# Kernel optimization log

Measured on AMD Instinct MI355X. Metric: run time of the kernel, lower is better.

## Reference

```python
import jax, jax.numpy as jnp
import numpy as np

DIM = 4096
NUM_HEAD = 32
NUM_KV_HEAD = 8
ROPE_THETA = 10000.0
B, T = 2, 2048


def apply_rope(x, start_pos=0, theta=ROPE_THETA):
    # x: [B, T, H, d_head]; rotate half-split pairs by position-dependent angles
    d = x.shape[-1]
    half = d // 2
    inv_freq = 1.0 / (theta ** (jnp.arange(0, half, dtype=jnp.float32) / half))
    pos = jnp.arange(x.shape[1], dtype=jnp.float32) + start_pos  # [T]
    ang = pos[:, None] * inv_freq[None, :]                       # [T, half]
    cos = jnp.cos(ang)[None, :, None, :]
    sin = jnp.sin(ang)[None, :, None, :]
    x1, x2 = x[..., :half], x[..., half:]
    return jnp.concatenate([x1 * cos - x2 * sin, x1 * sin + x2 * cos], axis=-1)


def setup_inputs() -> dict:
    key = jax.random.key(0)
    ks = jax.random.split(key, 5)
    scale = 0.02
    X = jax.random.normal(ks[0], (B, T, DIM), dtype=jnp.float32)
    Wq = jax.random.normal(ks[1], (DIM, DIM), dtype=jnp.float32) * scale
    Wk = jax.random.normal(ks[2], (DIM, DIM // NUM_HEAD * NUM_KV_HEAD), dtype=jnp.float32) * scale
    Wv = jax.random.normal(ks[3], (DIM, DIM // NUM_HEAD * NUM_KV_HEAD), dtype=jnp.float32) * scale
    Wo = jax.random.normal(ks[4], (DIM, DIM), dtype=jnp.float32) * scale
    return {"X": X, "Wq": Wq, "Wk": Wk, "Wv": Wv, "Wo": Wo}


def reference(X, Wq, Wk, Wv, Wo):
    Bs, Ts, C = X.shape
    H, Hkv = NUM_HEAD, NUM_KV_HEAD
    dh = C // H
    G = H // Hkv  # GQA group size

    Q = apply_rope((X @ Wq).reshape(Bs, Ts, H, dh))      # [B,T,H,dh]
    K = apply_rope((X @ Wk).reshape(Bs, Ts, Hkv, dh))    # [B,T,Hkv,dh]
    V = (X @ Wv).reshape(Bs, Ts, Hkv, dh)                # [B,T,Hkv,dh]

    # [B,Hkv,G,T,dh]: grouped layout equivalent to repeat_interleave on head dim
    Qh = Q.transpose(0, 2, 1, 3).reshape(Bs, Hkv, G, Ts, dh)
    Kh = K.transpose(0, 2, 1, 3)  # [B,Hkv,T,dh]
    Vh = V.transpose(0, 2, 1, 3)

    scores = jnp.einsum('bkgtd,bksd->bkgts', Qh, Kh) / jnp.sqrt(jnp.float32(dh))
    causal = jnp.tril(jnp.ones((Ts, Ts), dtype=bool))
    scores = jnp.where(causal[None, None, None], scores, -jnp.inf)
    attn = jax.nn.softmax(scores, axis=-1)
    out = jnp.einsum('bkgts,bksd->bkgtd', attn, Vh)       # [B,Hkv,G,T,dh]
    out = out.reshape(Bs, H, Ts, dh).transpose(0, 2, 1, 3).reshape(Bs, Ts, C)
    return out @ Wo
```

## Files before the change

kernel.cpp:

```cpp
#include <hip/hip_runtime.h>
#include <hip/hip_bf16.h>
#include <cstdint>
#include <cstddef>

#define B_   2
#define T_   2048
#define DIM_ 4096
#define H_   32
#define HKV_ 8
#define DH_  128
#define MROWS (B_*T_)

typedef __bf16 bf16_t;
typedef bf16_t bf16x8 __attribute__((ext_vector_type(8)));
typedef bf16_t bf16x4 __attribute__((ext_vector_type(4)));
typedef float  f32x4  __attribute__((ext_vector_type(4)));

typedef __attribute__((address_space(1))) void gvoid_t;
typedef __attribute__((address_space(3))) void lvoid_t;

__device__ __forceinline__ void gld_lds16(const void* g, void* l) {
  __builtin_amdgcn_global_load_lds((gvoid_t*)g, (lvoid_t*)l, 16, 0, 0);
}

__device__ __forceinline__ f32x4 mfma16(bf16x8 a, bf16x8 b, f32x4 c) {
  return __builtin_amdgcn_mfma_f32_16x16x32_bf16(a, b, c, 0, 0, 0);
}

__global__ void cast_f32_bf16(const float* __restrict__ in,
                              bf16_t* __restrict__ out, int n4) {
  int i = blockIdx.x * blockDim.x + threadIdx.x;
  if (i < n4) {
    float4 v = ((const float4*)in)[i];
    bf16x4 o;
    o[0] = (bf16_t)v.x; o[1] = (bf16_t)v.y; o[2] = (bf16_t)v.z; o[3] = (bf16_t)v.w;
    ((bf16x4*)out)[i] = o;
  }
}

__global__ void transpose_cast(const float* __restrict__ in,
                               bf16_t* __restrict__ out, int K, int N) {
  __shared__ float tile[32][33];
  int n0 = blockIdx.x * 32, k0 = blockIdx.y * 32;
  int tx = threadIdx.x, ty = threadIdx.y;
#pragma unroll
  for (int j = 0; j < 4; ++j)
    tile[ty + j*8][tx] = in[(size_t)(k0 + ty + j*8) * N + n0 + tx];
  __syncthreads();
#pragma unroll
  for (int j = 0; j < 4; ++j)
    out[(size_t)(n0 + ty + j*8) * K + k0 + tx] = (bf16_t)tile[tx][ty + j*8];
}

template <int OUT_F32>
__global__ __launch_bounds__(256, 2)
void gemm_bt(const bf16_t* __restrict__ A, const bf16_t* __restrict__ BT,
             void* __restrict__ C, int M, int N, int K) {
  __shared__ __align__(16) bf16_t Als[128 * 32];
  __shared__ __align__(16) bf16_t Bls[128 * 32];
  const int tid  = threadIdx.x;
  const int wave = tid >> 6, lane = tid & 63;
  const int quad = lane >> 4, l16 = lane & 15;
  const int wm = wave >> 1, wn = wave & 1;
  const int m0 = blockIdx.y * 128, n0 = blockIdx.x * 128;

  f32x4 acc[4][4] = {};

  const int srow = lane >> 2;
  const int scol = (lane & 3) * 8;

  for (int k0 = 0; k0 < K; k0 += 32) {
#pragma unroll
    for (int c = 0; c < 2; ++c) {
      int ch = wave * 2 + c;
      gld_lds16(A + (size_t)(m0 + ch*16 + srow) * K + k0 + scol,
                &Als[ch*512 + srow*32 + scol]);
    }
#pragma unroll
    for (int c = 0; c < 2; ++c) {
      int ch = wave * 2 + c;
      gld_lds16(BT + (size_t)(n0 + ch*16 + srow) * K + k0 + scol,
                &Bls[ch*512 + srow*32 + scol]);
    }
    __syncthreads();

    bf16x8 af[4], bfr[4];
#pragma unroll
    for (int mi = 0; mi < 4; ++mi)
      af[mi] = *(const bf16x8*)&Als[(wm*64 + mi*16 + l16)*32 + quad*8];
#pragma unroll
    for (int ni = 0; ni < 4; ++ni)
      bfr[ni] = *(const bf16x8*)&Bls[(wn*64 + ni*16 + l16)*32 + quad*8];
#pragma unroll
    for (int mi = 0; mi < 4; ++mi)
#pragma unroll
      for (int ni = 0; ni < 4; ++ni)
        acc[mi][ni] = mfma16(af[mi], bfr[ni], acc[mi][ni]);
    __syncthreads();
  }

#pragma unroll
  for (int mi = 0; mi < 4; ++mi)
#pragma unroll
    for (int ni = 0; ni < 4; ++ni)
#pragma unroll
      for (int r = 0; r < 4; ++r) {
        int row = m0 + wm*64 + mi*16 + quad*4 + r;
        int col = n0 + wn*64 + ni*16 + l16;
        if (OUT_F32)
          ((float*)C)[(size_t)row * N + col] = acc[mi][ni][r];
        else
          ((bf16_t*)C)[(size_t)row * N + col] = (bf16_t)acc[mi][ni][r];
      }
}

__global__ void rope_kernel(bf16_t* __restrict__ X, int Hn, int total) {
  int i = blockIdx.x * blockDim.x + threadIdx.x;
  if (i >= total) return;
  int d   = i & 63;
  int rem = i >> 6;
  int h   = rem % Hn; rem /= Hn;
  int t   = rem % T_;
  int b   = rem / T_;
  size_t base = ((size_t)(b * T_ + t) * Hn + h) * DH_;
  float x1 = (float)X[base + d];
  float x2 = (float)X[base + 64 + d];
  float inv_freq = expf(-(float)d * 0.14391156758f);
  float ang = (float)t * inv_freq;
  float s, c;
  sincosf(ang, &s, &c);
  X[base + d]      = (bf16_t)(x1 * c - x2 * s);
  X[base + 64 + d] = (bf16_t)(x1 * s + x2 * c);
}

__global__ void v_transpose(const bf16_t* __restrict__ Vb,
                            bf16_t* __restrict__ VT) {
  __shared__ bf16_t tile[32][33];
  int t0 = blockIdx.x * 32;
  int d0 = blockIdx.y * 32;
  int bk = blockIdx.z;
  int b = bk >> 3, kv = bk & 7;
  int tx = threadIdx.x, ty = threadIdx.y;
#pragma unroll
  for (int j = 0; j < 4; ++j)
    tile[ty + j*8][tx] =
        Vb[(size_t)(b * T_ + t0 + ty + j*8) * (HKV_*DH_) + kv*DH_ + d0 + tx];
  __syncthreads();
#pragma unroll
  for (int j = 0; j < 4; ++j)
    VT[((size_t)bk * DH_ + d0 + ty + j*8) * T_ + t0 + tx] = tile[tx][ty + j*8];
}

__global__ __launch_bounds__(256, 2)
void flash_attn(const bf16_t* __restrict__ Qb, const bf16_t* __restrict__ Kb,
                const bf16_t* __restrict__ VT, bf16_t* __restrict__ Ob) {
  __shared__ __align__(16) bf16_t Kls[2][64 * 128];
  __shared__ __align__(16) bf16_t Vls[2][128 * 64];
  __shared__ __align__(16) bf16_t Pls[128 * 64];

  const int tid = threadIdx.x, wave = tid >> 6, lane = tid & 63;
  const int quad = lane >> 4, l16 = lane & 15;
  const int qt = (int)gridDim.x - 1 - (int)blockIdx.x;
  const int h = blockIdx.y, b = blockIdx.z;
  const int kv = h >> 2;

  bf16x8 q[2][4];
#pragma unroll
  for (int mi = 0; mi < 2; ++mi) {
    const bf16_t* base =
        Qb + (size_t)(b*T_ + qt*128 + wave*32 + mi*16 + l16) * DIM_ + h*DH_;
#pragma unroll
    for (int kk = 0; kk < 4; ++kk)
      q[mi][kk] = *(const bf16x8*)(base + kk*32 + quad*8);
  }

  float m_st[2][4], l_st[2][4];
  f32x4 o_acc[2][8] = {};
#pragma unroll
  for (int mi = 0; mi < 2; ++mi)
#pragma unroll
    for (int r = 0; r < 4; ++r) { m_st[mi][r] = -1e30f; l_st[mi][r] = 0.f; }

  const int nkv = 2 * (qt + 1);

  auto stage = [&](int kvt, int pb) {
    int r_in = lane >> 4, cph = lane & 15;
#pragma unroll
    for (int c = 0; c < 4; ++c) {
      int ch = wave * 4 + c;
      int krow = ch * 4 + r_in;
      int clog = cph ^ (krow & 7);
      gld_lds16(Kb + (size_t)(b*T_ + kvt*64 + krow) * (HKV_*DH_) + kv*DH_ + clog*8,
                &Kls[pb][ch*512 + lane*8]);
    }
    int r8 = lane >> 3, c8 = lane & 7;
#pragma unroll
    for (int c = 0; c < 4; ++c) {
      int ch = wave * 4 + c;
      int drow = ch * 8 + r8;
      int clog = c8 ^ (drow & 7);
      gld_lds16(VT + ((size_t)(b*HKV_ + kv) * DH_ + drow) * T_ + kvt*64 + clog*8,
                &Vls[pb][ch*512 + lane*8]);
    }
  };

  stage(0, 0);

  const float S2 = 0.08838834764831845f * 1.4426950408889634f;
  const float THRraw = 8.0f / 0.08838834764831845f;

  for (int kvt = 0; kvt < nkv; ++kvt) {
    const int p = kvt & 1;
    __syncthreads();
    if (kvt + 1 < nkv) stage(kvt + 1, p ^ 1);

    f32x4 s[2][4] = {};
    __builtin_amdgcn_s_setprio(1);
#pragma unroll
    for (int kk = 0; kk < 4; ++kk) {
      bf16x8 kf[4];
#pragma unroll
      for (int ni = 0; ni < 4; ++ni) {
        int krow = ni*16 + l16;
        int cphys = (kk*4 + quad) ^ (krow & 7);
        kf[ni] = *(const bf16x8*)&Kls[p][krow*128 + cphys*8];
      }
#pragma unroll
      for (int mi = 0; mi < 2; ++mi)
#pragma unroll
        for (int ni = 0; ni < 4; ++ni)
          s[mi][ni] = mfma16(q[mi][kk], kf[ni], s[mi][ni]);
    }
    __builtin_amdgcn_s_setprio(0);

    const bool need_mask = (kvt >= 2*qt);
#pragma unroll
    for (int mi = 0; mi < 2; ++mi) {
      float mx[4];
#pragma unroll
      for (int r = 0; r < 4; ++r) {
        int rpos = qt*128 + wave*32 + mi*16 + quad*4 + r;
        float m = -1e30f;
#pragma unroll
        for (int ni = 0; ni < 4; ++ni) {
          float v = s[mi][ni][r];
          if (need_mask) {
            int cpos = kvt*64 + ni*16 + l16;
            if (cpos > rpos) v = -1e30f;
          }
          s[mi][ni][r] = v;
          m = fmaxf(m, v);
        }
#pragma unroll
        for (int off = 1; off < 16; off <<= 1)
          m = fmaxf(m, __shfl_xor(m, off, 64));
        mx[r] = m;
      }
      bool defer = true;
#pragma unroll
      for (int r = 0; r < 4; ++r)
        defer = defer && (mx[r] <= m_st[mi][r] + THRraw);
      if (__all(defer)) {
#pragma unroll
        for (int r = 0; r < 4; ++r) {
          float mn2 = m_st[mi][r] * S2;
          float rs = 0.f;
#pragma unroll
          for (int ni = 0; ni < 4; ++ni) {
            float pv = __builtin_amdgcn_exp2f(fmaf(s[mi][ni][r], S2, -mn2));
            s[mi][ni][r] = pv;
            rs += pv;
          }
#pragma unroll
          for (int off = 1; off < 16; off <<= 1)
            rs += __shfl_xor(rs, off, 64);
          l_st[mi][r] += rs;
        }
      } else {
        float al[4];
#pragma unroll
        for (int r = 0; r < 4; ++r) {
          float mnew = fmaxf(m_st[mi][r], mx[r]);
          al[r] = __builtin_amdgcn_exp2f((m_st[mi][r] - mnew) * S2);
          m_st[mi][r] = mnew;
          float mn2 = mnew * S2;
          float rs = 0.f;
#pragma unroll
          for (int ni = 0; ni < 4; ++ni) {
            float pv = __builtin_amdgcn_exp2f(fmaf(s[mi][ni][r], S2, -mn2));
            s[mi][ni][r] = pv;
            rs += pv;
          }
#pragma unroll
          for (int off = 1; off < 16; off <<= 1)
            rs += __shfl_xor(rs, off, 64);
          l_st[mi][r] = l_st[mi][r] * al[r] + rs;
        }
#pragma unroll
        for (int ni = 0; ni < 8; ++ni)
#pragma unroll
          for (int r = 0; r < 4; ++r) o_acc[mi][ni][r] *= al[r];
      }
#pragma unroll
      for (int ni = 0; ni < 4; ++ni)
#pragma unroll
        for (int r = 0; r < 4; ++r) {
          int prow = wave*32 + mi*16 + quad*4 + r;
          int g = (ni*2 + (l16 >> 3)) ^ (prow & 7);
          Pls[prow*64 + g*8 + (l16 & 7)] = (bf16_t)s[mi][ni][r];
        }
    }

    __builtin_amdgcn_s_setprio(1);
#pragma unroll
    for (int kk = 0; kk < 2; ++kk) {
      bf16x8 pf[2], vf[8];
#pragma unroll
      for (int mi = 0; mi < 2; ++mi) {
        int prow = wave*32 + mi*16 + l16;
        int g = (kk*4 + quad) ^ (prow & 7);
        pf[mi] = *(const bf16x8*)&Pls[prow*64 + g*8];
      }
#pragma unroll
      for (int ni = 0; ni < 8; ++ni) {
        int drow = ni*16 + l16;
        int cphys = (kk*4 + quad) ^ (drow & 7);
        vf[ni] = *(const bf16x8*)&Vls[p][drow*64 + cphys*8];
      }
#pragma unroll
      for (int mi = 0; mi < 2; ++mi)
#pragma unroll
        for (int ni = 0; ni < 8; ++ni)
          o_acc[mi][ni] = mfma16(pf[mi], vf[ni], o_acc[mi][ni]);
    }
    __builtin_amdgcn_s_setprio(0);
  }

#pragma unroll
  for (int mi = 0; mi < 2; ++mi) {
    float inv[4];
#pragma unroll
    for (int r = 0; r < 4; ++r) inv[r] = 1.f / l_st[mi][r];
#pragma unroll
    for (int ni = 0; ni < 8; ++ni)
#pragma unroll
      for (int r = 0; r < 4; ++r) {
        size_t row = (size_t)(b*T_ + qt*128 + wave*32 + mi*16 + quad*4 + r);
        int col = h*DH_ + ni*16 + l16;
        Ob[row * DIM_ + col] = (bf16_t)(o_acc[mi][ni][r] * inv[r]);
      }
  }
}

extern "C" void kernel_launch(void* const* d_in, const int* in_sizes, int n_in,
                              void* d_out, int out_size, void* d_ws, size_t ws_size,
                              hipStream_t stream) {
  const float* X  = (const float*)d_in[0];
  const float* Wq = (const float*)d_in[1];
  const float* Wk = (const float*)d_in[2];
  const float* Wv = (const float*)d_in[3];
  const float* Wo = (const float*)d_in[4];
  float* out = (float*)d_out;

  char* ws = (char*)d_ws;
  const size_t SZ_X  = (size_t)MROWS * DIM_ * 2;
  const size_t SZ_WQ = (size_t)DIM_ * DIM_ * 2;
  const size_t SZ_WK = (size_t)DIM_ * 1024 * 2;
  bf16_t* Xb  = (bf16_t*)(ws);
  bf16_t* WqT = (bf16_t*)(ws + SZ_X);
  bf16_t* WkT = (bf16_t*)(ws + SZ_X + SZ_WQ);
  bf16_t* WvT = (bf16_t*)(ws + SZ_X + SZ_WQ + SZ_WK);
  bf16_t* WoT = (bf16_t*)(ws + SZ_X + SZ_WQ + 2*SZ_WK);
  bf16_t* Qb  = (bf16_t*)(ws + SZ_X + 2*SZ_WQ + 2*SZ_WK);
  bf16_t* Kb  = (bf16_t*)(ws + 2*SZ_X + 2*SZ_WQ + 2*SZ_WK);
  bf16_t* Vb  = (bf16_t*)(ws + 2*SZ_X + 2*SZ_WQ + 3*SZ_WK);
  bf16_t* VT  = (bf16_t*)(ws + 2*SZ_X + 2*SZ_WQ + 4*SZ_WK);
  bf16_t* Ob  = Xb;

  {
    int n4 = MROWS * DIM_ / 4;
    cast_f32_bf16<<<(n4 + 255)/256, 256, 0, stream>>>(X, Xb, n4);
  }
  transpose_cast<<<dim3(DIM_/32, DIM_/32), dim3(32,8), 0, stream>>>(Wq, WqT, DIM_, DIM_);
  transpose_cast<<<dim3(1024/32, DIM_/32), dim3(32,8), 0, stream>>>(Wk, WkT, DIM_, 1024);
  transpose_cast<<<dim3(1024/32, DIM_/32), dim3(32,8), 0, stream>>>(Wv, WvT, DIM_, 1024);
  transpose_cast<<<dim3(DIM_/32, DIM_/32), dim3(32,8), 0, stream>>>(Wo, WoT, DIM_, DIM_);

  gemm_bt<0><<<dim3(DIM_/128, MROWS/128), 256, 0, stream>>>(Xb, WqT, Qb, MROWS, DIM_, DIM_);
  gemm_bt<0><<<dim3(1024/128, MROWS/128), 256, 0, stream>>>(Xb, WkT, Kb, MROWS, 1024, DIM_);
  gemm_bt<0><<<dim3(1024/128, MROWS/128), 256, 0, stream>>>(Xb, WvT, Vb, MROWS, 1024, DIM_);

  {
    int totq = B_ * T_ * H_ * 64;
    rope_kernel<<<(totq + 255)/256, 256, 0, stream>>>(Qb, H_, totq);
    int totk = B_ * T_ * HKV_ * 64;
    rope_kernel<<<(totk + 255)/256, 256, 0, stream>>>(Kb, HKV_, totk);
  }

  v_transpose<<<dim3(T_/32, DH_/32, B_*HKV_), dim3(32,8), 0, stream>>>(Vb, VT);

  flash_attn<<<dim3(T_/128, H_, B_), 256, 0, stream>>>(Qb, Kb, VT, Ob);

  gemm_bt<1><<<dim3(DIM_/128, MROWS/128), 256, 0, stream>>>(Ob, WoT, out, MROWS, DIM_, DIM_);
}
```

Before: 1.075 ms.

## Read K/V directly from global memory with XCD-aware GQA block mapping

Drops the double-buffered LDS staging of K and V tiles and their per-iteration barrier. Each wave now loads its K and V MMA fragments straight from global memory. The launch becomes a 1D grid, remapped so that all query heads and tiles sharing one KV head land on the same XCD and can reuse K/V through its L2. The P buffer gets a padded stride of 72 instead of an XOR swizzle. This trades LDS traffic and synchronisation for more global/L2 loads per wave, with some redundancy across waves in a block, and relies on L2 locality to keep those loads cheap.

```diff
diff --git a/kernel.cpp b/kernel.cpp
--- a/kernel.cpp
+++ b/kernel.cpp
@@ -154,15 +154,19 @@
 __global__ __launch_bounds__(256, 2)
 void flash_attn(const bf16_t* __restrict__ Qb, const bf16_t* __restrict__ Kb,
                 const bf16_t* __restrict__ VT, bf16_t* __restrict__ Ob) {
-  __shared__ __align__(16) bf16_t Kls[2][64 * 128];
-  __shared__ __align__(16) bf16_t Vls[2][128 * 64];
-  __shared__ __align__(16) bf16_t Pls[128 * 64];
+  __shared__ __align__(16) bf16_t Pls[128 * 72];
 
   const int tid = threadIdx.x, wave = tid >> 6, lane = tid & 63;
   const int quad = lane >> 4, l16 = lane & 15;
-  const int qt = (int)gridDim.x - 1 - (int)blockIdx.x;
-  const int h = blockIdx.y, b = blockIdx.z;
-  const int kv = h >> 2;
+
+  const int linear = blockIdx.x;
+  const int xcd  = linear & 7;
+  const int slot = linear >> 3;
+  const int g    = ((slot >> 6) << 3) + xcd;
+  const int b    = g >> 3, kv = g & 7;
+  const int j    = slot & 63;
+  const int qt   = 15 - (j >> 2);
+  const int h    = kv * 4 + (j & 3);
 
   bf16x8 q[2][4];
 #pragma unroll
@@ -182,56 +186,30 @@
     for (int r = 0; r < 4; ++r) { m_st[mi][r] = -1e30f; l_st[mi][r] = 0.f; }
 
   const int nkv = 2 * (qt + 1);
-
-  auto stage = [&](int kvt, int pb) {
-    int r_in = lane >> 4, cph = lane & 15;
-#pragma unroll
-    for (int c = 0; c < 4; ++c) {
-      int ch = wave * 4 + c;
-      int krow = ch * 4 + r_in;
-      int clog = cph ^ (krow & 7);
-      gld_lds16(Kb + (size_t)(b*T_ + kvt*64 + krow) * (HKV_*DH_) + kv*DH_ + clog*8,
-                &Kls[pb][ch*512 + lane*8]);
-    }
-    int r8 = lane >> 3, c8 = lane & 7;
-#pragma unroll
-    for (int c = 0; c < 4; ++c) {
-      int ch = wave * 4 + c;
-      int drow = ch * 8 + r8;
-      int clog = c8 ^ (drow & 7);
-      gld_lds16(VT + ((size_t)(b*HKV_ + kv) * DH_ + drow) * T_ + kvt*64 + clog*8,
-                &Vls[pb][ch*512 + lane*8]);
-    }
-  };
-
-  stage(0, 0);
-
   const float S2 = 0.08838834764831845f * 1.4426950408889634f;
   const float THRraw = 8.0f / 0.08838834764831845f;
 
+  const bf16_t* Kbase = Kb + (size_t)b * T_ * (HKV_*DH_) + kv * DH_;
+  const bf16_t* Vbase = VT + (size_t)(b*HKV_ + kv) * DH_ * T_;
+
   for (int kvt = 0; kvt < nkv; ++kvt) {
-    const int p = kvt & 1;
-    __syncthreads();
-    if (kvt + 1 < nkv) stage(kvt + 1, p ^ 1);
-
     f32x4 s[2][4] = {};
-    __builtin_amdgcn_s_setprio(1);
 #pragma unroll
     for (int kk = 0; kk < 4; ++kk) {
       bf16x8 kf[4];
 #pragma unroll
       for (int ni = 0; ni < 4; ++ni) {
-        int krow = ni*16 + l16;
-        int cphys = (kk*4 + quad) ^ (krow & 7);
-        kf[ni] = *(const bf16x8*)&Kls[p][krow*128 + cphys*8];
-      }
+        int krow = kvt*64 + ni*16 + l16;
+        kf[ni] = *(const bf16x8*)(Kbase + (size_t)krow * (HKV_*DH_) + kk*32 + quad*8);
+      }
+      __builtin_amdgcn_s_setprio(1);
 #pragma unroll
       for (int mi = 0; mi < 2; ++mi)
 #pragma unroll
         for (int ni = 0; ni < 4; ++ni)
           s[mi][ni] = mfma16(q[mi][kk], kf[ni], s[mi][ni]);
-    }
-    __builtin_amdgcn_s_setprio(0);
+      __builtin_amdgcn_s_setprio(0);
+    }
 
     const bool need_mask = (kvt >= 2*qt);
 #pragma unroll
@@ -306,34 +284,29 @@
 #pragma unroll
         for (int r = 0; r < 4; ++r) {
           int prow = wave*32 + mi*16 + quad*4 + r;
-          int g = (ni*2 + (l16 >> 3)) ^ (prow & 7);
-          Pls[prow*64 + g*8 + (l16 & 7)] = (bf16_t)s[mi][ni][r];
+          Pls[prow*72 + ni*16 + l16] = (bf16_t)s[mi][ni][r];
         }
     }
 
-    __builtin_amdgcn_s_setprio(1);
-#pragma unroll
-    for (int kk = 0; kk < 2; ++kk) {
-      bf16x8 pf[2], vf[8];
-#pragma unroll
-      for (int mi = 0; mi < 2; ++mi) {
-        int prow = wave*32 + mi*16 + l16;
-        int g = (kk*4 + quad) ^ (prow & 7);
-        pf[mi] = *(const bf16x8*)&Pls[prow*64 + g*8];
-      }
-#pragma unroll
-      for (int ni = 0; ni < 8; ++ni) {
-        int drow = ni*16 + l16;
-        int cphys = (kk*4 + quad) ^ (drow & 7);
-        vf[ni] = *(const bf16x8*)&Vls[p][drow*64 + cphys*8];
-      }
+    bf16x8 pf[2][2];
+#pragma unroll
+    for (int kk = 0; kk < 2; ++kk)
 #pragma unroll
       for (int mi = 0; mi < 2; ++mi)
-#pragma unroll
-        for (int ni = 0; ni < 8; ++ni)
-          o_acc[mi][ni] = mfma16(pf[mi], vf[ni], o_acc[mi][ni]);
-    }
-    __builtin_amdgcn_s_setprio(0);
+        pf[kk][mi] = *(const bf16x8*)&Pls[(wave*32 + mi*16 + l16)*72 + kk*32 + quad*8];
+#pragma unroll
+    for (int ni = 0; ni < 8; ++ni) {
+      int drow = ni*16 + l16;
+      const bf16_t* vb = Vbase + (size_t)drow * T_ + kvt*64;
+      bf16x8 va = *(const bf16x8*)(vb + quad*8);
+      bf16x8 vc = *(const bf16x8*)(vb + 32 + quad*8);
+      __builtin_amdgcn_s_setprio(1);
+      o_acc[0][ni] = mfma16(pf[0][0], va, o_acc[0][ni]);
+      o_acc[1][ni] = mfma16(pf[0][1], va, o_acc[1][ni]);
+      o_acc[0][ni] = mfma16(pf[1][0], vc, o_acc[0][ni]);
+      o_acc[1][ni] = mfma16(pf[1][1], vc, o_acc[1][ni]);
+      __builtin_amdgcn_s_setprio(0);
+    }
   }
 
 #pragma unroll
@@ -399,7 +372,7 @@
 
   v_transpose<<<dim3(T_/32, DH_/32, B_*HKV_), dim3(32,8), 0, stream>>>(Vb, VT);
 
-  flash_attn<<<dim3(T_/128, H_, B_), 256, 0, stream>>>(Qb, Kb, VT, Ob);
+  flash_attn<<<dim3((T_/128) * H_ * B_), 256, 0, stream>>>(Qb, Kb, VT, Ob);
 
   gemm_bt<1><<<dim3(DIM_/128, MROWS/128), 256, 0, stream>>>(Ob, WoT, out, MROWS, DIM_, DIM_);
 }
```

Result: faster. 989.3 us (-7.9%).
